# Kernel tuning notes

Hardware: AMD Instinct MI355X
Metric: run time of the kernel (lower is better)

## Reference

```python
import jax, jax.numpy as jnp
import numpy as np

B, C, S, E = 2, 4, 2048, 512
H, D, WIN = 8, 64, 256


def _local_windowed_attention(q, k, v, window):
    # q,k,v: [B,H,C,S,D]; causal sliding window of size `window` (keys i-window+1..i)
    b, h, c, s, d = q.shape
    nb = s // window  # S must be divisible by window
    qb = q.reshape(b, h, c, nb, window, d)
    pad = jnp.zeros((b, h, c, 1, window, d), q.dtype)
    kb = jnp.concatenate([pad, k.reshape(b, h, c, nb, window, d)], axis=3)
    vb = jnp.concatenate([pad, v.reshape(b, h, c, nb, window, d)], axis=3)
    # each query block attends to [previous block, own block] -> 2*window keys
    k2 = jnp.concatenate([kb[:, :, :, :-1], kb[:, :, :, 1:]], axis=4)  # [b,h,c,nb,2w,d]
    v2 = jnp.concatenate([vb[:, :, :, :-1], vb[:, :, :, 1:]], axis=4)
    j = jnp.arange(nb)
    qpos = j[:, None] * window + jnp.arange(window)[None, :]              # [nb, w]
    kpos = (j[:, None] - 1) * window + jnp.arange(2 * window)[None, :]    # [nb, 2w]
    diff = qpos[:, :, None] - kpos[:, None, :]                            # [nb, w, 2w]
    mask = (diff >= 0) & (diff < window)  # causal + window; also kills the zero-padding block (j=0)
    scale = 1.0 / np.sqrt(d)
    scores = jnp.einsum('bhcnqd,bhcnkd->bhcnqk', qb, k2) * scale
    scores = jnp.where(mask[None, None, None], scores, jnp.asarray(-1e30, scores.dtype))
    attn = jax.nn.softmax(scores, axis=-1)
    ctx = jnp.einsum('bhcnqk,bhcnkd->bhcnqd', attn, v2)
    return ctx.reshape(b, h, c, s, d)


def setup_inputs() -> dict:
    key = jax.random.key(0)
    ks = jax.random.split(key, 8)
    w_scale = np.sqrt(6.0 / (E + E))  # xavier_uniform for square Linear
    def xav(k):
        return jax.random.uniform(k, (E, E), jnp.float32, -w_scale, w_scale)
    return {
        'query': jax.random.normal(ks[0], (B, C, S, E), jnp.float32),
        'key': jax.random.normal(ks[1], (B, C, S, E), jnp.float32),
        'value': jax.random.normal(ks[2], (B, C, S, E), jnp.float32),
        'Wq': xav(ks[3]), 'bq': jnp.zeros((E,), jnp.float32),
        'Wk': xav(ks[4]), 'bk': jnp.zeros((E,), jnp.float32),
        'Wv': xav(ks[5]), 'bv': jnp.zeros((E,), jnp.float32),
        'Wo': xav(ks[6]), 'bo': jnp.zeros((E,), jnp.float32),
    }


def reference(query, key, value, Wq, bq, Wk, bk, Wv, bv, Wo, bo):
    b, c, s, e = query.shape
    q = query @ Wq.T + bq
    k = key @ Wk.T + bk
    v = value @ Wv.T + bv
    # [b,c,s,e] -> [b,h,c,s,d]
    def split_heads(x):
        return x.reshape(b, c, s, H, D).transpose(0, 3, 1, 2, 4)
    ctx = _local_windowed_attention(split_heads(q), split_heads(k), split_heads(v), WIN)
    # [b,h,c,s,d] -> [b,c,s,e]
    ctx = ctx.transpose(0, 2, 3, 1, 4).reshape(b, c, s, e)
    out = ctx @ Wo.T + bo
    return out
```

## Files before the change

kernel.cpp:

```cpp
#include <hip/hip_runtime.h>
#include <hip/hip_bf16.h>


typedef __bf16 bf16x8 __attribute__((ext_vector_type(8)));
typedef float f32x4 __attribute__((ext_vector_type(4)));
typedef unsigned short u16x8 __attribute__((ext_vector_type(8)));

#define GLDS(gp, lp) __builtin_amdgcn_global_load_lds( \
    (const __attribute__((address_space(1))) void*)(gp), \
    (__attribute__((address_space(3))) void*)(lp), 16, 0, 0)

__device__ __forceinline__ unsigned short f2bf(float f) {
  unsigned u = __float_as_uint(f);
  return (unsigned short)((u + 0x7fffu + ((u >> 16) & 1u)) >> 16);
}

__global__ void convert_all(const float* __restrict__ q, const float* __restrict__ k,
                            const float* __restrict__ v,
                            const float* __restrict__ wq, const float* __restrict__ wk,
                            const float* __restrict__ wv, const float* __restrict__ wo,
                            unsigned short* __restrict__ dq, unsigned short* __restrict__ dk,
                            unsigned short* __restrict__ dv,
                            unsigned short* __restrict__ dwq, unsigned short* __restrict__ dwk,
                            unsigned short* __restrict__ dwv, unsigned short* __restrict__ dwo) {
  int z = blockIdx.z;
  const float* s;
  unsigned short* d;
  long long i;
  if (z < 3) {
    s = z == 0 ? q : z == 1 ? k : v;
    d = z == 0 ? dq : z == 1 ? dk : dv;
    i = ((long long)blockIdx.x * 256 + threadIdx.x) * 8;
  } else {
    int x = blockIdx.x;
    if (x >= 512) return;
    int wi = x >> 7;
    s = wi == 0 ? wq : wi == 1 ? wk : wi == 2 ? wv : wo;
    d = wi == 0 ? dwq : wi == 1 ? dwk : wi == 2 ? dwv : dwo;
    i = ((long long)(x & 127) * 256 + threadIdx.x) * 8;
  }
  f32x4 a = *reinterpret_cast<const f32x4*>(s + i);
  f32x4 b = *reinterpret_cast<const f32x4*>(s + i + 4);
  u16x8 o;
  o[0] = f2bf(a[0]); o[1] = f2bf(a[1]); o[2] = f2bf(a[2]); o[3] = f2bf(a[3]);
  o[4] = f2bf(b[0]); o[5] = f2bf(b[1]); o[6] = f2bf(b[2]); o[7] = f2bf(b[3]);
  *reinterpret_cast<u16x8*>(d + i) = o;
}

__global__ __launch_bounds__(256, 3)
void gemm_qkv(const unsigned short* __restrict__ Xq, const unsigned short* __restrict__ Xk,
              const unsigned short* __restrict__ Xv,
              const unsigned short* __restrict__ wq, const unsigned short* __restrict__ wk,
              const unsigned short* __restrict__ wv,
              const float* __restrict__ bq, const float* __restrict__ bk,
              const float* __restrict__ bv,
              unsigned short* __restrict__ qout, unsigned short* __restrict__ kout,
              unsigned short* __restrict__ vtout) {
  __shared__ char lds_raw[33280];
  const int z = blockIdx.z;
  const unsigned short* A  = z == 0 ? Xq : z == 1 ? Xk : Xv;
  const unsigned short* Bw = z == 0 ? wq : z == 1 ? wk : wv;
  const float* bias        = z == 0 ? bq : z == 1 ? bk : bv;

  unsigned short* Alds = (unsigned short*)lds_raw;
  unsigned short* Blds = (unsigned short*)(lds_raw + 16384);
  const int t = threadIdx.x;
  const int l = t & 63, w = t >> 6;
  const int lrow = l & 15, lk = l >> 4;
  const int rbase = blockIdx.y * 128, cbase = blockIdx.x * 128;
  const int wm = w >> 1, wn = w & 1;
  f32x4 acc[4][4] = {};

  for (int k0 = 0; k0 < 512; k0 += 64) {
    __syncthreads();
#pragma unroll
    for (int i = 0; i < 4; ++i) {
      int byteoff = w * 4096 + i * 1024;
      int row = w * 32 + i * 8 + (l >> 3);
      int chunk = l & 7;
      GLDS(A + (size_t)(rbase + row) * 512 + k0 + chunk * 8, lds_raw + byteoff);
      GLDS(Bw + (size_t)(cbase + row) * 512 + k0 + chunk * 8, lds_raw + 16384 + byteoff);
    }
    __syncthreads();
    bf16x8 af[4][2], bfr[4][2];
#pragma unroll
    for (int mt = 0; mt < 4; ++mt)
#pragma unroll
      for (int ks = 0; ks < 2; ++ks) {
        af[mt][ks]  = *reinterpret_cast<const bf16x8*>(Alds + (wm * 64 + mt * 16 + lrow) * 64 + ks * 32 + lk * 8);
        bfr[mt][ks] = *reinterpret_cast<const bf16x8*>(Blds + (wn * 64 + mt * 16 + lrow) * 64 + ks * 32 + lk * 8);
      }
#pragma unroll
    for (int mt = 0; mt < 4; ++mt)
#pragma unroll
      for (int nt = 0; nt < 4; ++nt) {
        acc[mt][nt] = __builtin_amdgcn_mfma_f32_16x16x32_bf16(af[mt][0], bfr[nt][0], acc[mt][nt], 0, 0, 0);
        acc[mt][nt] = __builtin_amdgcn_mfma_f32_16x16x32_bf16(af[mt][1], bfr[nt][1], acc[mt][nt], 0, 0, 0);
      }
  }

  float bvv[4];
#pragma unroll
  for (int nt = 0; nt < 4; ++nt) bvv[nt] = bias[cbase + wn * 64 + nt * 16 + lrow];

  if (z < 2) {
    unsigned short* out = z == 0 ? qout : kout;
#pragma unroll
    for (int mt = 0; mt < 4; ++mt)
#pragma unroll
      for (int nt = 0; nt < 4; ++nt)
#pragma unroll
        for (int r = 0; r < 4; ++r) {
          int rg = rbase + wm * 64 + mt * 16 + lk * 4 + r;
          int cg = cbase + wn * 64 + nt * 16 + lrow;
          out[(size_t)rg * 512 + cg] = f2bf(acc[mt][nt][r] + bvv[nt]);
        }
  } else {
    __syncthreads();
    unsigned short* tl = (unsigned short*)lds_raw;
#pragma unroll
    for (int mt = 0; mt < 4; ++mt)
#pragma unroll
      for (int nt = 0; nt < 4; ++nt)
#pragma unroll
        for (int r = 0; r < 4; ++r)
          tl[(wm * 64 + mt * 16 + lk * 4 + r) * 130 + wn * 64 + nt * 16 + lrow] =
              f2bf(acc[mt][nt][r] + bvv[nt]);
    __syncthreads();
    const int bc = rbase >> 11;
    const int sb = rbase & 2047;
#pragma unroll
    for (int rnd = 0; rnd < 8; ++rnd) {
      int idx = rnd * 256 + t;
      int el = idx >> 4;
      int ch = idx & 15;
      u16x8 pk;
#pragma unroll
      for (int j2 = 0; j2 < 8; ++j2) pk[j2] = tl[(ch * 8 + j2) * 130 + el];
      int eg = cbase + el;
      int hh = eg >> 6, dd = eg & 63;
      *reinterpret_cast<u16x8*>(vtout + ((size_t)(bc * 8 + hh) * 64 + dd) * 2048 + sb + ch * 8) = pk;
    }
  }
}

__global__ __launch_bounds__(256, 3)
void gemm_out(const unsigned short* __restrict__ A, const unsigned short* __restrict__ Bw,
              const float* __restrict__ bias, float* __restrict__ out) {
  __shared__ char lds_raw[32768];
  unsigned short* Alds = (unsigned short*)lds_raw;
  unsigned short* Blds = (unsigned short*)(lds_raw + 16384);
  const int t = threadIdx.x;
  const int l = t & 63, w = t >> 6;
  const int lrow = l & 15, lk = l >> 4;
  const int rbase = blockIdx.y * 128, cbase = blockIdx.x * 128;
  const int wm = w >> 1, wn = w & 1;
  f32x4 acc[4][4] = {};

  for (int k0 = 0; k0 < 512; k0 += 64) {
    __syncthreads();
#pragma unroll
    for (int i = 0; i < 4; ++i) {
      int byteoff = w * 4096 + i * 1024;
      int row = w * 32 + i * 8 + (l >> 3);
      int chunk = l & 7;
      GLDS(A + (size_t)(rbase + row) * 512 + k0 + chunk * 8, lds_raw + byteoff);
      GLDS(Bw + (size_t)(cbase + row) * 512 + k0 + chunk * 8, lds_raw + 16384 + byteoff);
    }
    __syncthreads();
    bf16x8 af[4][2], bfr[4][2];
#pragma unroll
    for (int mt = 0; mt < 4; ++mt)
#pragma unroll
      for (int ks = 0; ks < 2; ++ks) {
        af[mt][ks]  = *reinterpret_cast<const bf16x8*>(Alds + (wm * 64 + mt * 16 + lrow) * 64 + ks * 32 + lk * 8);
        bfr[mt][ks] = *reinterpret_cast<const bf16x8*>(Blds + (wn * 64 + mt * 16 + lrow) * 64 + ks * 32 + lk * 8);
      }
#pragma unroll
    for (int mt = 0; mt < 4; ++mt)
#pragma unroll
      for (int nt = 0; nt < 4; ++nt) {
        acc[mt][nt] = __builtin_amdgcn_mfma_f32_16x16x32_bf16(af[mt][0], bfr[nt][0], acc[mt][nt], 0, 0, 0);
        acc[mt][nt] = __builtin_amdgcn_mfma_f32_16x16x32_bf16(af[mt][1], bfr[nt][1], acc[mt][nt], 0, 0, 0);
      }
  }

  float bvv[4];
#pragma unroll
  for (int nt = 0; nt < 4; ++nt) bvv[nt] = bias[cbase + wn * 64 + nt * 16 + lrow];
#pragma unroll
  for (int mt = 0; mt < 4; ++mt)
#pragma unroll
    for (int nt = 0; nt < 4; ++nt)
#pragma unroll
      for (int r = 0; r < 4; ++r) {
        int rg = rbase + wm * 64 + mt * 16 + lk * 4 + r;
        int cg = cbase + wn * 64 + nt * 16 + lrow;
        out[(size_t)rg * 512 + cg] = acc[mt][nt][r] + bvv[nt];
      }
}

__global__ __launch_bounds__(256, 3)
void attn_kernel(const unsigned short* __restrict__ qm, const unsigned short* __restrict__ km,
                 const unsigned short* __restrict__ vtm, unsigned short* __restrict__ ctx) {
  __shared__ char lds_raw[49152];
  const int t = threadIdx.x, l = t & 63, w = t >> 6;
  char* Plds = lds_raw + 32768 + w * 4096;
  const int lrow = l & 15, lk = l >> 4;

  int flat = blockIdx.x + 16 * (blockIdx.y + 8 * blockIdx.z);
  int swz = (flat & 7) * 128 + (flat >> 3);
  const int jh = swz & 15, h = (swz >> 4) & 7, bc = swz >> 7;

  const int Qb = jh * 128;
  const int qlo = Qb + w * 32;
  const int h64 = h * 64;
  const size_t bcrow = (size_t)bc * 2048;
  const size_t bch64 = ((size_t)(bc * 8 + h)) * 64;

  const int tlo = (Qb > 255 ? Qb - 255 : 0) >> 6;
  const int thi = (Qb + 127) >> 6;
  const int nt = thi - tlo + 1;
  const int wlo = (qlo > 255 ? qlo - 255 : 0) >> 6;
  const int whi = (qlo + 31) >> 6;

  auto stage = [&](int tt, int buf) {
    char* Kb = lds_raw + buf * 16384;
#pragma unroll
    for (int i = 0; i < 2; ++i) {
      int byteoff = w * 2048 + i * 1024;
      int row = w * 16 + i * 8 + (l >> 3);
      int clog = (l & 7) ^ (row & 7);
      GLDS(km + (bcrow + tt * 64 + row) * 512 + h64 + clog * 8, Kb + byteoff);
      GLDS(vtm + (bch64 + row) * 2048 + tt * 64 + clog * 8, Kb + 8192 + byteoff);
    }
  };

  bf16x8 qf[2][2];
#pragma unroll
  for (int rt = 0; rt < 2; ++rt)
#pragma unroll
    for (int ks = 0; ks < 2; ++ks)
      qf[rt][ks] = *reinterpret_cast<const bf16x8*>(
          qm + (bcrow + qlo + rt * 16 + lrow) * 512 + h64 + ks * 32 + lk * 8);

  f32x4 oacc[2][4] = {};
  float ms[2][4], ls[2][4];
#pragma unroll
  for (int rt = 0; rt < 2; ++rt)
#pragma unroll
    for (int r = 0; r < 4; ++r) { ms[rt][r] = -INFINITY; ls[rt][r] = 0.f; }

  stage(tlo, 0);
  __syncthreads();

  for (int it = 0; it < nt; ++it) {
    const int tt = tlo + it;
    if (it + 1 < nt) stage(tt + 1, (it + 1) & 1);

    if (tt >= wlo && tt <= whi) {
      char* Kb = lds_raw + (it & 1) * 16384;
      char* Vb = Kb + 8192;

      f32x4 sc[2][4];
      f32x4 zero = {};
#pragma unroll
      for (int kt = 0; kt < 4; ++kt) {
        int krow = kt * 16 + lrow;
        const char* kbase = Kb + krow * 128;
        bf16x8 kf0 = *reinterpret_cast<const bf16x8*>(kbase + ((lk ^ (krow & 7)) << 4));
        bf16x8 kf1 = *reinterpret_cast<const bf16x8*>(kbase + (((4 + lk) ^ (krow & 7)) << 4));
#pragma unroll
        for (int rt = 0; rt < 2; ++rt) {
          f32x4 s0 = __builtin_amdgcn_mfma_f32_16x16x32_bf16(qf[rt][0], kf0, zero, 0, 0, 0);
          sc[rt][kt] = __builtin_amdgcn_mfma_f32_16x16x32_bf16(qf[rt][1], kf1, s0, 0, 0, 0);
        }
      }

      float tmax[2][4];
#pragma unroll
      for (int rt = 0; rt < 2; ++rt)
#pragma unroll
        for (int r = 0; r < 4; ++r) tmax[rt][r] = -1e30f;
#pragma unroll
      for (int rt = 0; rt < 2; ++rt)
#pragma unroll
        for (int kt = 0; kt < 4; ++kt)
#pragma unroll
          for (int r = 0; r < 4; ++r) {
            int p = qlo + rt * 16 + lk * 4 + r;
            int kk = tt * 64 + kt * 16 + lrow;
            bool ok = (kk <= p) && (kk + 255 >= p);
            float sv = ok ? sc[rt][kt][r] * 0.125f : -1e30f;
            sc[rt][kt][r] = sv;
            tmax[rt][r] = fmaxf(tmax[rt][r], sv);
          }
#pragma unroll
      for (int rt = 0; rt < 2; ++rt)
#pragma unroll
        for (int r = 0; r < 4; ++r) {
#pragma unroll
          for (int dx = 1; dx < 16; dx <<= 1)
            tmax[rt][r] = fmaxf(tmax[rt][r], __shfl_xor(tmax[rt][r], dx, 64));
          float mnew = fmaxf(ms[rt][r], tmax[rt][r]);
          float corr = __expf(ms[rt][r] - mnew);
          ms[rt][r] = mnew;
          ls[rt][r] *= corr;
#pragma unroll
          for (int dt = 0; dt < 4; ++dt) oacc[rt][dt][r] *= corr;
        }

      float psum[2][4] = {};
#pragma unroll
      for (int rt = 0; rt < 2; ++rt)
#pragma unroll
        for (int kt = 0; kt < 4; ++kt)
#pragma unroll
          for (int r = 0; r < 4; ++r) {
            int p_ = qlo + rt * 16 + lk * 4 + r;
            int kk = tt * 64 + kt * 16 + lrow;
            bool ok = (kk <= p_) && (kk + 255 >= p_);
            float pv = ok ? __expf(sc[rt][kt][r] - ms[rt][r]) : 0.f;
            psum[rt][r] += pv;
            int prow = rt * 16 + lk * 4 + r;
            int pcol = kt * 16 + lrow;
            *reinterpret_cast<unsigned short*>(
                Plds + prow * 128 + (((pcol >> 3) ^ (prow & 7)) << 4) + (pcol & 7) * 2) = f2bf(pv);
          }
#pragma unroll
      for (int rt = 0; rt < 2; ++rt)
#pragma unroll
        for (int r = 0; r < 4; ++r) {
#pragma unroll
          for (int dx = 1; dx < 16; dx <<= 1)
            psum[rt][r] += __shfl_xor(psum[rt][r], dx, 64);
          ls[rt][r] += psum[rt][r];
        }

#pragma unroll
      for (int ks = 0; ks < 2; ++ks) {
        bf16x8 pa[2], vb[4];
#pragma unroll
        for (int rt = 0; rt < 2; ++rt) {
          int row = rt * 16 + lrow;
          int c = ks * 4 + lk;
          pa[rt] = *reinterpret_cast<const bf16x8*>(Plds + row * 128 + ((c ^ (row & 7)) << 4));
        }
#pragma unroll
        for (int dt = 0; dt < 4; ++dt) {
          int row = dt * 16 + lrow;
          int c = ks * 4 + lk;
          vb[dt] = *reinterpret_cast<const bf16x8*>(Vb + row * 128 + ((c ^ (row & 7)) << 4));
        }
#pragma unroll
        for (int rt = 0; rt < 2; ++rt)
#pragma unroll
          for (int dt = 0; dt < 4; ++dt)
            oacc[rt][dt] = __builtin_amdgcn_mfma_f32_16x16x32_bf16(pa[rt], vb[dt], oacc[rt][dt], 0, 0, 0);
      }
    }
    __syncthreads();
  }

  if (qlo < 255) {
#pragma unroll
    for (int rt = 0; rt < 2; ++rt)
#pragma unroll
      for (int r = 0; r < 4; ++r) {
        int p = qlo + rt * 16 + lk * 4 + r;
        float cp = (float)(255 - p > 0 ? 255 - p : 0);
        float m = ms[rt][r];
        float mn = cp > 0.f ? fmaxf(m, 0.f) : m;
        float sc0 = __expf(m - mn);
        ls[rt][r] = ls[rt][r] * sc0 + cp * __expf(-mn);
#pragma unroll
        for (int dt = 0; dt < 4; ++dt) oacc[rt][dt][r] *= sc0;
      }
  }

#pragma unroll
  for (int rt = 0; rt < 2; ++rt)
#pragma unroll
    for (int r = 0; r < 4; ++r) {
      float inv = 1.f / ls[rt][r];
#pragma unroll
      for (int dt = 0; dt < 4; ++dt) {
        size_t rg = bcrow + qlo + rt * 16 + lk * 4 + r;
        int cg = h64 + dt * 16 + lrow;
        ctx[rg * 512 + cg] = f2bf(oacc[rt][dt][r] * inv);
      }
    }
}

extern "C" void kernel_launch(void* const* d_in, const int* in_sizes, int n_in,
                              void* d_out, int out_size, void* d_ws, size_t ws_size,
                              hipStream_t stream) {
  const float* q_in = (const float*)d_in[0];
  const float* k_in = (const float*)d_in[1];
  const float* v_in = (const float*)d_in[2];
  const float* Wq = (const float*)d_in[3];
  const float* bq = (const float*)d_in[4];
  const float* Wk = (const float*)d_in[5];
  const float* bk = (const float*)d_in[6];
  const float* Wv = (const float*)d_in[7];
  const float* bv = (const float*)d_in[8];
  const float* Wo = (const float*)d_in[9];
  const float* bo = (const float*)d_in[10];

  char* ws = (char*)d_ws;
  const size_t SZ = (size_t)16384 * 512 * 2;
  unsigned short* Xq = (unsigned short*)(ws);
  unsigned short* Xk = (unsigned short*)(ws + SZ);
  unsigned short* Xv = (unsigned short*)(ws + 2 * SZ);
  unsigned short* qb = (unsigned short*)(ws + 3 * SZ);
  unsigned short* kb = (unsigned short*)(ws + 4 * SZ);
  unsigned short* wq_b = (unsigned short*)(ws + 5 * SZ);
  unsigned short* wk_b = wq_b + 262144;
  unsigned short* wv_b = wk_b + 262144;
  unsigned short* wo_b = wv_b + 262144;
  unsigned short* vtb = (unsigned short*)d_out;
  unsigned short* ctx = Xq;

  convert_all<<<dim3(4096, 1, 4), 256, 0, stream>>>(q_in, k_in, v_in, Wq, Wk, Wv, Wo,
                                                    Xq, Xk, Xv, wq_b, wk_b, wv_b, wo_b);
  gemm_qkv<<<dim3(4, 128, 3), 256, 0, stream>>>(Xq, Xk, Xv, wq_b, wk_b, wv_b,
                                                bq, bk, bv, qb, kb, vtb);
  attn_kernel<<<dim3(16, 8, 8), 256, 0, stream>>>(qb, kb, vtb, ctx);
  gemm_out<<<dim3(4, 128), 256, 0, stream>>>(ctx, wo_b, bo, (float*)d_out);
}
```

Before: 277.1 us.

## Drop online max in windowed attention, transpose score MFMA, pack P stores

```diff
diff --git a/kernel.cpp b/kernel.cpp
--- a/kernel.cpp
+++ b/kernel.cpp
@@ -5,6 +5,7 @@
 typedef __bf16 bf16x8 __attribute__((ext_vector_type(8)));
 typedef float f32x4 __attribute__((ext_vector_type(4)));
 typedef unsigned short u16x8 __attribute__((ext_vector_type(8)));
+typedef unsigned int u32x2 __attribute__((ext_vector_type(2)));
 
 #define GLDS(gp, lp) __builtin_amdgcn_global_load_lds( \
     (const __attribute__((address_space(1))) void*)(gp), \
@@ -200,15 +201,15 @@
       }
 }
 
-__global__ __launch_bounds__(256, 3)
+__global__ __launch_bounds__(256, 4)
 void attn_kernel(const unsigned short* __restrict__ qm, const unsigned short* __restrict__ km,
                  const unsigned short* __restrict__ vtm, unsigned short* __restrict__ ctx) {
-  __shared__ char lds_raw[49152];
+  __shared__ char lds_raw[40960];
   const int t = threadIdx.x, l = t & 63, w = t >> 6;
-  char* Plds = lds_raw + 32768 + w * 4096;
-  const int lrow = l & 15, lk = l >> 4;
-
-  int flat = blockIdx.x + 16 * (blockIdx.y + 8 * blockIdx.z);
+  char* Pl = lds_raw + 32768 + w * 2048;
+  const int lm = l & 15, g = l >> 4;
+
+  int flat = blockIdx.x;
   int swz = (flat & 7) * 128 + (flat >> 3);
   const int jh = swz & 15, h = (swz >> 4) & 7, bc = swz >> 7;
 
@@ -242,14 +243,10 @@
 #pragma unroll
     for (int ks = 0; ks < 2; ++ks)
       qf[rt][ks] = *reinterpret_cast<const bf16x8*>(
-          qm + (bcrow + qlo + rt * 16 + lrow) * 512 + h64 + ks * 32 + lk * 8);
+          qm + (bcrow + qlo + rt * 16 + lm) * 512 + h64 + ks * 32 + g * 8);
 
   f32x4 oacc[2][4] = {};
-  float ms[2][4], ls[2][4];
-#pragma unroll
-  for (int rt = 0; rt < 2; ++rt)
-#pragma unroll
-    for (int r = 0; r < 4; ++r) { ms[rt][r] = -INFINITY; ls[rt][r] = 0.f; }
+  float ls[2] = {0.f, 0.f};
 
   stage(tlo, 0);
   __syncthreads();
@@ -266,91 +263,71 @@
       f32x4 zero = {};
 #pragma unroll
       for (int kt = 0; kt < 4; ++kt) {
-        int krow = kt * 16 + lrow;
+        int krow = kt * 16 + lm;
         const char* kbase = Kb + krow * 128;
-        bf16x8 kf0 = *reinterpret_cast<const bf16x8*>(kbase + ((lk ^ (krow & 7)) << 4));
-        bf16x8 kf1 = *reinterpret_cast<const bf16x8*>(kbase + (((4 + lk) ^ (krow & 7)) << 4));
+        bf16x8 kf0 = *reinterpret_cast<const bf16x8*>(kbase + ((g ^ (krow & 7)) << 4));
+        bf16x8 kf1 = *reinterpret_cast<const bf16x8*>(kbase + (((4 + g) ^ (krow & 7)) << 4));
 #pragma unroll
         for (int rt = 0; rt < 2; ++rt) {
-          f32x4 s0 = __builtin_amdgcn_mfma_f32_16x16x32_bf16(qf[rt][0], kf0, zero, 0, 0, 0);
-          sc[rt][kt] = __builtin_amdgcn_mfma_f32_16x16x32_bf16(qf[rt][1], kf1, s0, 0, 0, 0);
+          f32x4 s0 = __builtin_amdgcn_mfma_f32_16x16x32_bf16(kf0, qf[rt][0], zero, 0, 0, 0);
+          sc[rt][kt] = __builtin_amdgcn_mfma_f32_16x16x32_bf16(kf1, qf[rt][1], s0, 0, 0, 0);
         }
       }
 
-      float tmax[2][4];
-#pragma unroll
-      for (int rt = 0; rt < 2; ++rt)
-#pragma unroll
-        for (int r = 0; r < 4; ++r) tmax[rt][r] = -1e30f;
-#pragma unroll
-      for (int rt = 0; rt < 2; ++rt)
-#pragma unroll
-        for (int kt = 0; kt < 4; ++kt)
-#pragma unroll
-          for (int r = 0; r < 4; ++r) {
-            int p = qlo + rt * 16 + lk * 4 + r;
-            int kk = tt * 64 + kt * 16 + lrow;
-            bool ok = (kk <= p) && (kk + 255 >= p);
-            float sv = ok ? sc[rt][kt][r] * 0.125f : -1e30f;
-            sc[rt][kt][r] = sv;
-            tmax[rt][r] = fmaxf(tmax[rt][r], sv);
+      const bool interior = (tt * 64 + 63 <= qlo) && (tt * 64 >= qlo + 31 - 255);
+      if (interior) {
+#pragma unroll
+        for (int rt = 0; rt < 2; ++rt) {
+          float acc = 0.f;
+#pragma unroll
+          for (int kt = 0; kt < 4; ++kt)
+#pragma unroll
+            for (int r = 0; r < 4; ++r) {
+              float pv = __expf(sc[rt][kt][r] * 0.125f);
+              sc[rt][kt][r] = pv;
+              acc += pv;
+            }
+          ls[rt] += acc;
+        }
+      } else {
+#pragma unroll
+        for (int rt = 0; rt < 2; ++rt) {
+          int d0 = qlo + rt * 16 + lm - (tt * 64 + g * 4);
+          float acc = 0.f;
+#pragma unroll
+          for (int kt = 0; kt < 4; ++kt)
+#pragma unroll
+            for (int r = 0; r < 4; ++r) {
+              bool ok = (unsigned)(d0 - (kt * 16 + r)) <= 255u;
+              float pv = ok ? __expf(sc[rt][kt][r] * 0.125f) : 0.f;
+              sc[rt][kt][r] = pv;
+              acc += pv;
+            }
+          ls[rt] += acc;
+        }
+      }
+
+#pragma unroll
+      for (int ks = 0; ks < 2; ++ks) {
+#pragma unroll
+        for (int rt = 0; rt < 2; ++rt)
+#pragma unroll
+          for (int ktl = 0; ktl < 2; ++ktl) {
+            int kt = ks * 2 + ktl;
+            unsigned u0, u1;
+            asm("v_cvt_pk_bf16_f32 %0, %1, %2" : "=v"(u0) : "v"(sc[rt][kt][0]), "v"(sc[rt][kt][1]));
+            asm("v_cvt_pk_bf16_f32 %0, %1, %2" : "=v"(u1) : "v"(sc[rt][kt][2]), "v"(sc[rt][kt][3]));
+            u32x2 uu; uu[0] = u0; uu[1] = u1;
+            *reinterpret_cast<u32x2*>(Pl + (rt * 16 + lm) * 64 + ktl * 32 + g * 8) = uu;
           }
-#pragma unroll
-      for (int rt = 0; rt < 2; ++rt)
-#pragma unroll
-        for (int r = 0; r < 4; ++r) {
-#pragma unroll
-          for (int dx = 1; dx < 16; dx <<= 1)
-            tmax[rt][r] = fmaxf(tmax[rt][r], __shfl_xor(tmax[rt][r], dx, 64));
-          float mnew = fmaxf(ms[rt][r], tmax[rt][r]);
-          float corr = __expf(ms[rt][r] - mnew);
-          ms[rt][r] = mnew;
-          ls[rt][r] *= corr;
-#pragma unroll
-          for (int dt = 0; dt < 4; ++dt) oacc[rt][dt][r] *= corr;
-        }
-
-      float psum[2][4] = {};
-#pragma unroll
-      for (int rt = 0; rt < 2; ++rt)
-#pragma unroll
-        for (int kt = 0; kt < 4; ++kt)
-#pragma unroll
-          for (int r = 0; r < 4; ++r) {
-            int p_ = qlo + rt * 16 + lk * 4 + r;
-            int kk = tt * 64 + kt * 16 + lrow;
-            bool ok = (kk <= p_) && (kk + 255 >= p_);
-            float pv = ok ? __expf(sc[rt][kt][r] - ms[rt][r]) : 0.f;
-            psum[rt][r] += pv;
-            int prow = rt * 16 + lk * 4 + r;
-            int pcol = kt * 16 + lrow;
-            *reinterpret_cast<unsigned short*>(
-                Plds + prow * 128 + (((pcol >> 3) ^ (prow & 7)) << 4) + (pcol & 7) * 2) = f2bf(pv);
-          }
-#pragma unroll
-      for (int rt = 0; rt < 2; ++rt)
-#pragma unroll
-        for (int r = 0; r < 4; ++r) {
-#pragma unroll
-          for (int dx = 1; dx < 16; dx <<= 1)
-            psum[rt][r] += __shfl_xor(psum[rt][r], dx, 64);
-          ls[rt][r] += psum[rt][r];
-        }
-
-#pragma unroll
-      for (int ks = 0; ks < 2; ++ks) {
-        bf16x8 pa[2], vb[4];
-#pragma unroll
-        for (int rt = 0; rt < 2; ++rt) {
-          int row = rt * 16 + lrow;
-          int c = ks * 4 + lk;
-          pa[rt] = *reinterpret_cast<const bf16x8*>(Plds + row * 128 + ((c ^ (row & 7)) << 4));
-        }
+        bf16x8 pa[2];
+        pa[0] = *reinterpret_cast<const bf16x8*>(Pl + lm * 64 + g * 16);
+        pa[1] = *reinterpret_cast<const bf16x8*>(Pl + (16 + lm) * 64 + g * 16);
+        bf16x8 vb[4];
 #pragma unroll
         for (int dt = 0; dt < 4; ++dt) {
-          int row = dt * 16 + lrow;
-          int c = ks * 4 + lk;
-          vb[dt] = *reinterpret_cast<const bf16x8*>(Vb + row * 128 + ((c ^ (row & 7)) << 4));
+          int vrow = dt * 16 + lm;
+          vb[dt] = *reinterpret_cast<const bf16x8*>(Vb + vrow * 128 + (((ks * 4 + g) ^ (vrow & 7)) << 4));
         }
 #pragma unroll
         for (int rt = 0; rt < 2; ++rt)
@@ -362,34 +339,34 @@
     __syncthreads();
   }
 
-  if (qlo < 255) {
-#pragma unroll
-    for (int rt = 0; rt < 2; ++rt)
+#pragma unroll
+  for (int rt = 0; rt < 2; ++rt) {
+    ls[rt] += __shfl_xor(ls[rt], 16, 64);
+    ls[rt] += __shfl_xor(ls[rt], 32, 64);
+    int cp = 255 - (qlo + rt * 16 + lm);
+    if (cp > 0) ls[rt] += (float)cp;
+  }
+
+  float* Pf = (float*)Pl;
+  Pf[lm] = 1.f / ls[0];
+  Pf[16 + lm] = 1.f / ls[1];
+  float inv0[2][4];
+#pragma unroll
+  for (int rt = 0; rt < 2; ++rt)
+#pragma unroll
+    for (int r = 0; r < 4; ++r)
+      inv0[rt][r] = Pf[rt * 16 + g * 4 + r];
+
+#pragma unroll
+  for (int rt = 0; rt < 2; ++rt)
+#pragma unroll
+    for (int dt = 0; dt < 4; ++dt)
 #pragma unroll
       for (int r = 0; r < 4; ++r) {
-        int p = qlo + rt * 16 + lk * 4 + r;
-        float cp = (float)(255 - p > 0 ? 255 - p : 0);
-        float m = ms[rt][r];
-        float mn = cp > 0.f ? fmaxf(m, 0.f) : m;
-        float sc0 = __expf(m - mn);
-        ls[rt][r] = ls[rt][r] * sc0 + cp * __expf(-mn);
-#pragma unroll
-        for (int dt = 0; dt < 4; ++dt) oacc[rt][dt][r] *= sc0;
-      }
-  }
-
-#pragma unroll
-  for (int rt = 0; rt < 2; ++rt)
-#pragma unroll
-    for (int r = 0; r < 4; ++r) {
-      float inv = 1.f / ls[rt][r];
-#pragma unroll
-      for (int dt = 0; dt < 4; ++dt) {
-        size_t rg = bcrow + qlo + rt * 16 + lk * 4 + r;
-        int cg = h64 + dt * 16 + lrow;
-        ctx[rg * 512 + cg] = f2bf(oacc[rt][dt][r] * inv);
-      }
-    }
+        size_t rg = bcrow + qlo + rt * 16 + g * 4 + r;
+        int cg = h64 + dt * 16 + lm;
+        ctx[rg * 512 + cg] = f2bf(oacc[rt][dt][r] * inv0[rt][r]);
+      }
 }
 
 extern "C" void kernel_launch(void* const* d_in, const int* in_sizes, int n_in,
@@ -425,6 +402,6 @@
                                                     Xq, Xk, Xv, wq_b, wk_b, wv_b, wo_b);
   gemm_qkv<<<dim3(4, 128, 3), 256, 0, stream>>>(Xq, Xk, Xv, wq_b, wk_b, wv_b,
                                                 bq, bk, bv, qb, kb, vtb);
-  attn_kernel<<<dim3(16, 8, 8), 256, 0, stream>>>(qb, kb, vtb, ctx);
+  attn_kernel<<<1024, 256, 0, stream>>>(qb, kb, vtb, ctx);
   gemm_out<<<dim3(4, 128), 256, 0, stream>>>(ctx, wo_b, bo, (float*)d_out);
 }
```

After: 250.2 us. 9.7% less time.
